# Optimization experiments

Hardware: AMD Instinct MI355X
Metric: run time of the kernel (lower is better)

The kernel has to match this reference:

```python
import jax, jax.numpy as jnp
import numpy as np

# Acoustic FDTD constants (seistorch-style geometry)
NSHOTS, NT = 4, 512
NZ, NX = 256, 256
NRECS = 128
DT = 1e-3   # s
DH = 10.0   # m grid spacing


def setup_inputs() -> dict:
    key = jax.random.key(0)
    k1, k2, k3, k4, k5, k6 = jax.random.split(key, 6)
    x = jax.random.normal(k1, (NSHOTS, NT), dtype=jnp.float32)  # source wavelets
    # velocity model in [1500, 4000] m/s (CFL: dt*vmax/dh = 0.4 < stability limit)
    vp = 1500.0 + 2500.0 * jax.random.uniform(k2, (NZ, NX), dtype=jnp.float32)
    src_z = jax.random.randint(k3, (NSHOTS,), 0, NZ)
    src_x = jax.random.randint(k4, (NSHOTS,), 0, NX)
    rec_z = jax.random.randint(k5, (NSHOTS, NRECS), 0, NZ)
    rec_x = jax.random.randint(k6, (NSHOTS, NRECS), 0, NX)
    return {"x": x, "vp": vp, "src_z": src_z, "src_x": src_x,
            "rec_z": rec_z, "rec_x": rec_x}


def _laplacian(p):
    # 5-point stencil, zero Dirichlet boundary. p: (B, NZ, NX)
    pp = jnp.pad(p, ((0, 0), (1, 1), (1, 1)))
    return (pp[:, 2:, 1:-1] + pp[:, :-2, 1:-1]
            + pp[:, 1:-1, 2:] + pp[:, 1:-1, :-2]
            - 4.0 * p) / (DH * DH)


def reference(x, vp, src_z, src_x, rec_z, rec_x):
    shots = jnp.arange(NSHOTS)
    c2dt2 = (vp * DT) ** 2  # (NZ, NX), broadcast over shots

    def step(carry, wav_t):
        p_prev, p = carry
        # 2nd-order acoustic update (the PDE "cell")
        p_next = 2.0 * p - p_prev + c2dt2 * _laplacian(p)
        # source scatter-inject (super_source)
        p_next = p_next.at[shots, src_z, src_x].add(wav_t * DT * DT)
        # receiver gather (super_probes): (NSHOTS, NRECS)
        rec = p_next[shots[:, None], rec_z, rec_x]
        return (p, p_next), rec

    p0 = jnp.zeros((NSHOTS, NZ, NX), dtype=x.dtype)
    _, recs = jax.lax.scan(step, (p0, p0), x.T)  # recs: (NT, NSHOTS, NRECS)
    # (shots, time, receivers, n_receiver_types=1)
    return jnp.transpose(recs, (1, 0, 2))[..., None]
```

## Files before the change

### kernel.cpp

```cpp
#include <hip/hip_runtime.h>

#define NSHOTS 4
#define NT     512
#define NZ     256
#define NX     256
#define NRECS  128

static constexpr float DTf    = 0.001f;
static constexpr float INVDH2 = 1.0f / (10.0f * 10.0f);

#define KSTEPS 16
#define TILE   32
#define RPT    8
#define NWAVES 8
#define BLOCK  512
#define NWG    (NSHOTS * 64)
#define NPHASE (NT / KSTEPS)
#define LSTRIDE 32

__device__ __forceinline__ float nbr_left(float v) {
  return __int_as_float(__builtin_amdgcn_update_dpp(
      0, __float_as_int(v), 0x138 , 0xf, 0xf, false));
}
__device__ __forceinline__ float nbr_right(float v) {
  return __int_as_float(__builtin_amdgcn_update_dpp(
      0, __float_as_int(v), 0x130 , 0xf, 0xf, false));
}

__device__ __forceinline__ float gload(const float* p) {
  return __hip_atomic_load(p, __ATOMIC_RELAXED, __HIP_MEMORY_SCOPE_AGENT);
}
__device__ __forceinline__ void gstore(float* p, float v) {
  __hip_atomic_store(p, v, __ATOMIC_RELAXED, __HIP_MEMORY_SCOPE_AGENT);
}
__device__ __forceinline__ unsigned fload(const unsigned* p) {
  return __hip_atomic_load(p, __ATOMIC_RELAXED, __HIP_MEMORY_SCOPE_AGENT);
}
__device__ __forceinline__ void fstore(unsigned* p, unsigned v) {
  __hip_atomic_store(p, v, __ATOMIC_RELAXED, __HIP_MEMORY_SCOPE_AGENT);
}

__global__ __launch_bounds__(BLOCK, 4) void wave_p2p(
    float* __restrict__ f0c, float* __restrict__ f0p,
    float* __restrict__ f1c, float* __restrict__ f1p,
    const float* __restrict__ vp, const float* __restrict__ xwav,
    const int* __restrict__ src_z, const int* __restrict__ src_x,
    const int* __restrict__ rec_z, const int* __restrict__ rec_x,
    float* __restrict__ out,
    unsigned* __restrict__ bar)
{
  const int bid  = blockIdx.x;
  const int s    = bid >> 6;
  const int tz   = (bid >> 3) & 7;
  const int tx   = bid & 7;
  const int tid  = threadIdx.x;
  const int w    = tid >> 6;
  const int lane = tid & 63;

  const int gz0 = tz * TILE - KSTEPS;
  const int gx0 = tx * TILE - KSTEPS;
  const int gx  = gx0 + lane;
  const int zb  = w * RPT;

  __shared__ float haloTop[2][NWAVES][64];
  __shared__ float haloBot[2][NWAVES][64];
  __shared__ float recTile[2][TILE][TILE + 1];
  __shared__ int   cntS;
  __shared__ int   lzA[NRECS], lxA[NRECS];
  __shared__ unsigned pkA[NRECS];

  if (tid == 0) cntS = 0;
  __syncthreads();
  if (tid < NRECS) {
    const int lz = rec_z[s * NRECS + tid] - tz * TILE;
    const int lx = rec_x[s * NRECS + tid] - tx * TILE;
    lzA[tid] = lz; lxA[tid] = lx;
    if ((unsigned)lz < (unsigned)TILE && (unsigned)lx < (unsigned)TILE) {
      const int k = atomicAdd(&cntS, 1);
      pkA[k] = (unsigned)tid | ((unsigned)lz << 8) | ((unsigned)lx << 16);
    }
  }
  __syncthreads();
  const int nRec = cntS;
  int myR = 0, myLz = 0, myLx = 0;
  if (tid < nRec) {
    const unsigned p = pkA[tid];
    myR = p & 255; myLz = (p >> 8) & 31; myLx = (p >> 16) & 31;
  }
  const bool wbRow = (w >= 2 && w < 6) && (lane >= KSTEPS && lane < KSTEPS + TILE);
  const int  ilz   = (w - 2) * RPT;
  const int  ilx   = lane - KSTEPS;
  unsigned recMask = 0;
  if (wbRow) {
    for (int r = 0; r < NRECS; ++r)
      if (lxA[r] == ilx && (unsigned)(lzA[r] - ilz) < (unsigned)RPT)
        recMask |= 1u << (lzA[r] - ilz);
  }

  int nb = -1;
  if (tid < 8) {
    const int k  = (tid < 4) ? tid : tid + 1;
    const int dz = k / 3 - 1, dx = k % 3 - 1;
    const int qz = tz + dz, qx = tx + dx;
    if ((unsigned)qz < 8u && (unsigned)qx < 8u)
      nb = (s << 6) | (qz << 3) | qx;
  }
  unsigned* wF = bar;
  unsigned* rF = bar + (size_t)NWG * LSTRIDE;

  auto pollGE = [&](unsigned* base, unsigned target) {
    if (nb >= 0) {
      while (fload(base + (size_t)nb * LSTRIDE) < target)
        __builtin_amdgcn_s_sleep(1);
    }
  };

  const int slz = src_z[s] - gz0;
  const int slx = src_x[s] - gx0;
  const bool srcMine = (slx == lane) && ((unsigned)(slz - zb) < (unsigned)RPT);
  const int  srcI = slz - zb;
  float srcM[RPT];
  #pragma unroll
  for (int i = 0; i < RPT; ++i) srcM[i] = (srcMine && srcI == i) ? 1.0f : 0.0f;

  const bool xok = (unsigned)gx < (unsigned)NX;
  float a[RPT], b[RPT], c2[RPT];
  #pragma unroll
  for (int i = 0; i < RPT; ++i) {
    const int gz = gz0 + zb + i;
    const bool ok = xok && ((unsigned)gz < (unsigned)NZ);
    float v = ok ? vp[gz * NX + gx] : 0.0f;
    v *= DTf;
    c2[i] = v * v * INVDH2;
    a[i] = 0.0f; b[i] = 0.0f;
  }

  #pragma unroll 1
  for (int ph = 0; ph < NPHASE; ++ph) {
    const int t0 = ph * KSTEPS;

    if (ph > 0) {
      pollGE(wF, (unsigned)ph);
      __syncthreads();
      const float* rc = (ph & 1) ? f0c : f1c;
      const float* rp = (ph & 1) ? f0p : f1p;
      if (!wbRow) {
        #pragma unroll
        for (int i = 0; i < RPT; ++i) {
          const int gz = gz0 + zb + i;
          const bool ok = xok && ((unsigned)gz < (unsigned)NZ);
          const int fidx = (s * NZ + gz) * NX + gx;
          a[i] = ok ? gload(rc + fidx) : 0.0f;
          b[i] = ok ? gload(rp + fidx) : 0.0f;
        }
      }
      __builtin_amdgcn_s_waitcnt(0);
      __syncthreads();
      if (tid == 0) fstore(rF + (size_t)bid * LSTRIDE, (unsigned)ph);
    }

    float amp[KSTEPS];
    #pragma unroll
    for (int t = 0; t < KSTEPS; ++t)
      amp[t] = (xwav[s * NT + t0 + t] * DTf) * DTf;

    float recv[KSTEPS];

    auto do_step = [&](float (&cur)[RPT], float (&nxt)[RPT], int tau) {
      const int pb = tau & 1;
      haloTop[pb][w][lane] = cur[0];
      haloBot[pb][w][lane] = cur[RPT - 1];
      __syncthreads();
      if (tau > 0 && tid < nRec) recv[tau - 1] = recTile[1 - pb][myLz][myLx];
      const float up0 = (w > 0)          ? haloBot[pb][w - 1][lane] : 0.0f;
      const float dn7 = (w < NWAVES - 1) ? haloTop[pb][w + 1][lane] : 0.0f;
      #pragma unroll
      for (int i = 0; i < RPT; ++i) {
        const float c  = cur[i];
        const float up = (i == 0)       ? up0 : cur[i - 1];
        const float dn = (i == RPT - 1) ? dn7 : cur[i + 1];
        const float lf = nbr_left(c);
        const float rt = nbr_right(c);
        const float sum = (up + dn) + (lf + rt);
        const float lap = __builtin_fmaf(-4.0f, c, sum);
        float v = __builtin_fmaf(2.0f, c, -nxt[i]);
        v = __builtin_fmaf(c2[i], lap, v);
        v = __builtin_fmaf(srcM[i], amp[tau], v);
        nxt[i] = v;
      }
      if (recMask) {
        #pragma unroll
        for (int i = 0; i < RPT; ++i)
          if (recMask & (1u << i)) recTile[pb][ilz + i][ilx] = nxt[i];
      }
    };

    #pragma unroll
    for (int h = 0; h < KSTEPS / 2; ++h) {
      do_step(a, b, 2 * h);
      do_step(b, a, 2 * h + 1);
    }

    if (ph >= 2 && ph != NPHASE - 1) pollGE(rF, (unsigned)(ph - 1));
    __syncthreads();
    if (tid < nRec) recv[KSTEPS - 1] = recTile[1][myLz][myLx];

    if (tid < nRec) {
      #pragma unroll
      for (int t = 0; t < KSTEPS; ++t)
        out[(s * NT + (t0 + t)) * NRECS + myR] = recv[t];
    }

    if (ph != NPHASE - 1) {
      float* wc = (ph & 1) ? f1c : f0c;
      float* wp = (ph & 1) ? f1p : f0p;
      if (wbRow) {
        #pragma unroll
        for (int i = 0; i < RPT; ++i) {
          const int gz = gz0 + zb + i;
          const int fidx = (s * NZ + gz) * NX + gx;
          gstore(wc + fidx, a[i]);
          gstore(wp + fidx, b[i]);
        }
      }
      __builtin_amdgcn_s_waitcnt(0);
      __syncthreads();
      if (tid == 0) fstore(wF + (size_t)bid * LSTRIDE, (unsigned)(ph + 1));
    }
  }
}

extern "C" void kernel_launch(void* const* d_in, const int* in_sizes, int n_in,
                              void* d_out, int out_size, void* d_ws, size_t ws_size,
                              hipStream_t stream) {
  const float* x     = (const float*)d_in[0];
  const float* vp    = (const float*)d_in[1];
  const int*   src_z = (const int*)d_in[2];
  const int*   src_x = (const int*)d_in[3];
  const int*   rec_z = (const int*)d_in[4];
  const int*   rec_x = (const int*)d_in[5];
  float* out = (float*)d_out;

  float* ws = (float*)d_ws;
  const size_t F = (size_t)NSHOTS * NZ * NX;
  float* f0c = ws;
  float* f0p = ws + F;
  float* f1c = ws + 2 * F;
  float* f1p = ws + 3 * F;
  unsigned* bar = (unsigned*)(ws + 4 * F);

  hipMemsetAsync(bar, 0, 2 * (size_t)NWG * LSTRIDE * sizeof(unsigned), stream);

  wave_p2p<<<dim3(NWG), dim3(BLOCK), 0, stream>>>(
      f0c, f0p, f1c, f1p, vp, x, src_z, src_x, rec_z, rec_x, out, bar);
}
```

Baseline: 366.7 us.

## Use four rotating field buffers to relax write-after-read neighbor polling

Replaces the double-buffered field exchange with a ring of four buffer pairs, so a block only has to wait for neighbors to have read a buffer from three phases back instead of the previous phase before overwriting it. This is meant to cut stalls on the read-flag barrier between neighboring workgroups. It also precomputes per-row global offsets and loads the source wavelet with float4 vector loads. The cost is twice the workspace, which assumes the harness provides enough scratch memory.

```diff
diff --git a/kernel.cpp b/kernel.cpp
--- a/kernel.cpp
+++ b/kernel.cpp
@@ -16,7 +16,9 @@
 #define BLOCK  512
 #define NWG    (NSHOTS * 64)
 #define NPHASE (NT / KSTEPS)
+#define NPAIR  4
 #define LSTRIDE 32
+#define FCNT   (NSHOTS * NZ * NX)
 
 __device__ __forceinline__ float nbr_left(float v) {
   return __int_as_float(__builtin_amdgcn_update_dpp(
@@ -40,9 +42,8 @@
   __hip_atomic_store(p, v, __ATOMIC_RELAXED, __HIP_MEMORY_SCOPE_AGENT);
 }
 
-__global__ __launch_bounds__(BLOCK, 4) void wave_p2p(
-    float* __restrict__ f0c, float* __restrict__ f0p,
-    float* __restrict__ f1c, float* __restrict__ f1p,
+__global__ __launch_bounds__(BLOCK, 4) void wave_p2p4(
+    float* __restrict__ fld,
     const float* __restrict__ vp, const float* __restrict__ xwav,
     const int* __restrict__ src_z, const int* __restrict__ src_x,
     const int* __restrict__ rec_z, const int* __restrict__ rec_x,
@@ -124,11 +125,15 @@
   for (int i = 0; i < RPT; ++i) srcM[i] = (srcMine && srcI == i) ? 1.0f : 0.0f;
 
   const bool xok = (unsigned)gx < (unsigned)NX;
+  int   offRow[RPT];
+  bool  okRow[RPT];
   float a[RPT], b[RPT], c2[RPT];
   #pragma unroll
   for (int i = 0; i < RPT; ++i) {
     const int gz = gz0 + zb + i;
     const bool ok = xok && ((unsigned)gz < (unsigned)NZ);
+    okRow[i]  = ok;
+    offRow[i] = ok ? ((s * NZ + gz) * NX + gx) : 0;
     float v = ok ? vp[gz * NX + gx] : 0.0f;
     v *= DTf;
     c2[i] = v * v * INVDH2;
@@ -142,16 +147,13 @@
     if (ph > 0) {
       pollGE(wF, (unsigned)ph);
       __syncthreads();
-      const float* rc = (ph & 1) ? f0c : f1c;
-      const float* rp = (ph & 1) ? f0p : f1p;
+      const float* rc = fld + (size_t)(((ph - 1) & (NPAIR - 1)) * 2) * FCNT;
+      const float* rp = rc + FCNT;
       if (!wbRow) {
         #pragma unroll
         for (int i = 0; i < RPT; ++i) {
-          const int gz = gz0 + zb + i;
-          const bool ok = xok && ((unsigned)gz < (unsigned)NZ);
-          const int fidx = (s * NZ + gz) * NX + gx;
-          a[i] = ok ? gload(rc + fidx) : 0.0f;
-          b[i] = ok ? gload(rp + fidx) : 0.0f;
+          a[i] = okRow[i] ? gload(rc + offRow[i]) : 0.0f;
+          b[i] = okRow[i] ? gload(rp + offRow[i]) : 0.0f;
         }
       }
       __builtin_amdgcn_s_waitcnt(0);
@@ -160,9 +162,17 @@
     }
 
     float amp[KSTEPS];
-    #pragma unroll
-    for (int t = 0; t < KSTEPS; ++t)
-      amp[t] = (xwav[s * NT + t0 + t] * DTf) * DTf;
+    {
+      const float4* xw4 = (const float4*)(xwav + s * NT + t0);
+      #pragma unroll
+      for (int q = 0; q < KSTEPS / 4; ++q) {
+        const float4 v = xw4[q];
+        amp[4 * q + 0] = (v.x * DTf) * DTf;
+        amp[4 * q + 1] = (v.y * DTf) * DTf;
+        amp[4 * q + 2] = (v.z * DTf) * DTf;
+        amp[4 * q + 3] = (v.w * DTf) * DTf;
+      }
+    }
 
     float recv[KSTEPS];
 
@@ -201,7 +211,7 @@
       do_step(b, a, 2 * h + 1);
     }
 
-    if (ph >= 2 && ph != NPHASE - 1) pollGE(rF, (unsigned)(ph - 1));
+    if (ph >= NPAIR && ph != NPHASE - 1) pollGE(rF, (unsigned)(ph - (NPAIR - 1)));
     __syncthreads();
     if (tid < nRec) recv[KSTEPS - 1] = recTile[1][myLz][myLx];
 
@@ -212,15 +222,13 @@
     }
 
     if (ph != NPHASE - 1) {
-      float* wc = (ph & 1) ? f1c : f0c;
-      float* wp = (ph & 1) ? f1p : f0p;
+      float* wc = fld + (size_t)((ph & (NPAIR - 1)) * 2) * FCNT;
+      float* wp = wc + FCNT;
       if (wbRow) {
         #pragma unroll
         for (int i = 0; i < RPT; ++i) {
-          const int gz = gz0 + zb + i;
-          const int fidx = (s * NZ + gz) * NX + gx;
-          gstore(wc + fidx, a[i]);
-          gstore(wp + fidx, b[i]);
+          gstore(wc + offRow[i], a[i]);
+          gstore(wp + offRow[i], b[i]);
         }
       }
       __builtin_amdgcn_s_waitcnt(0);
@@ -242,15 +250,11 @@
   float* out = (float*)d_out;
 
   float* ws = (float*)d_ws;
-  const size_t F = (size_t)NSHOTS * NZ * NX;
-  float* f0c = ws;
-  float* f0p = ws + F;
-  float* f1c = ws + 2 * F;
-  float* f1p = ws + 3 * F;
-  unsigned* bar = (unsigned*)(ws + 4 * F);
+  float* fld = ws;
+  unsigned* bar = (unsigned*)(ws + (size_t)NPAIR * 2 * FCNT);
 
   hipMemsetAsync(bar, 0, 2 * (size_t)NWG * LSTRIDE * sizeof(unsigned), stream);
 
-  wave_p2p<<<dim3(NWG), dim3(BLOCK), 0, stream>>>(
-      f0c, f0p, f1c, f1p, vp, x, src_z, src_x, rec_z, rec_x, out, bar);
-}
+  wave_p2p4<<<dim3(NWG), dim3(BLOCK), 0, stream>>>(
+      fld, vp, x, src_z, src_x, rec_z, rec_x, out, bar);
+}
```

New measurement: 390.2 us. 6.4% more time.
